# Kernel tuning notes

Hardware: AMD Instinct MI355X
Metric: run time of the kernel (lower is better)

## Reference

```python
import jax, jax.numpy as jnp
import numpy as np

NUM_CLASSES = 21
CHANNELS = 256


def setup_inputs() -> dict:
    key = jax.random.key(0)
    k1, k2 = jax.random.split(key)
    B, C, Hf, Wf = 16, CHANNELS, 128, 128
    Hl, Wl = 512, 512
    features = jax.random.normal(k1, (B, C, Hf, Wf), dtype=jnp.float32)
    labels = jax.random.randint(k2, (B, Hl, Wl), 0, NUM_CLASSES, dtype=jnp.int64)
    return {"features": features, "labels": labels}


def _nearest_resize_labels(labels, Hf, Wf):
    # torch F.interpolate(mode='nearest'): src = floor(dst * in/out)
    B, Hl, Wl = labels.shape
    ih = (jnp.arange(Hf) * Hl) // Hf  # [Hf]
    iw = (jnp.arange(Wf) * Wl) // Wf  # [Wf]
    return labels[:, ih[:, None], iw[None, :]]  # [B, Hf, Wf]


def reference(features, labels):
    B, C, Hf, Wf = features.shape
    lab = _nearest_resize_labels(labels, Hf, Wf)  # [B,Hf,Wf] int
    seg = lab.reshape(-1)  # [B*Hf*Wf]
    feats = features.transpose(0, 2, 3, 1).reshape(-1, C)  # [B*Hf*Wf, C]
    # segment-mean over classes: sums and counts in one fused pass each
    sums = jax.ops.segment_sum(feats, seg, num_segments=NUM_CLASSES)  # [K, C]
    counts = jax.ops.segment_sum(jnp.ones((seg.shape[0],), dtype=feats.dtype), seg,
                                 num_segments=NUM_CLASSES)  # [K]
    protos = sums / jnp.maximum(counts, 1.0)[:, None]
    # classes absent from the batch produce no proto (dict omission in the original);
    # represent as zeros here, with counts signalling validity
    protos = jnp.where(counts[:, None] > 0, protos, jnp.zeros_like(protos))
    return protos, counts
```

## Files before the change

kernel.cpp:

```cpp
#include <hip/hip_runtime.h>
#include <hip/hip_bf16.h>

#define NUM_CLASSES 21
#define CHANNELS 256
#define B_SZ 16
#define HF 128
#define WF 128
#define HL 512
#define WL 512
#define PIX_PER_BLOCK 512
#define TILES_PER_B (HF * WF / PIX_PER_BLOCK)
#define PCHUNK 64
#define NCHUNK (PIX_PER_BLOCK / PCHUNK)
#define FPAD 65

__global__ __launch_bounds__(256) void protos_accum_kernel(
    const float* __restrict__ feats,
    const int*   __restrict__ labels,
    float* __restrict__ sums,
    int*   __restrict__ counts)
{
    __shared__ float fbuf[CHANNELS * FPAD];
    __shared__ int   lbl[PIX_PER_BLOCK];
    __shared__ int   cnt[NUM_CLASSES];

    const int t    = threadIdx.x;
    const int lane = t & 63;
    const int b    = blockIdx.x >> 5;
    const int tile = blockIdx.x & 31;
    const int base = tile * PIX_PER_BLOCK;

    if (t < NUM_CLASSES) cnt[t] = 0;

    const int p0 = base + 2 * t;
    const int h0 = p0 >> 7,       w0 = p0 & 127;
    const int h1 = (p0 + 1) >> 7, w1 = (p0 + 1) & 127;
    const int l0 = labels[(size_t)b * (HL * WL) + (size_t)(h0 * 4) * WL + w0 * 4];
    const int l1 = labels[(size_t)b * (HL * WL) + (size_t)(h1 * 4) * WL + w1 * 4];
    lbl[2 * t]     = l0;
    lbl[2 * t + 1] = l1;
    __syncthreads();
    atomicAdd(&cnt[l0], 1);
    atomicAdd(&cnt[l1], 1);

    float acc[NUM_CLASSES];
    #pragma unroll
    for (int k = 0; k < NUM_CLASSES; ++k) acc[k] = 0.0f;

    const float* fb = feats + (size_t)b * CHANNELS * (HF * WF);

    for (int chk = 0; chk < NCHUNK; ++chk) {
        const int pbase = base + chk * PCHUNK;

        float4 v[16];
        #pragma unroll
        for (int i = 0; i < 16; ++i) {
            const int flat = i * 256 + t;
            const int c = flat >> 4;
            const int q = flat & 15;
            v[i] = *(const float4*)(fb + (size_t)c * (HF * WF) + pbase + q * 4);
        }
        __syncthreads();

        #pragma unroll
        for (int i = 0; i < 16; ++i) {
            const int flat = i * 256 + t;
            const int c = flat >> 4;
            const int q = flat & 15;
            float* d = &fbuf[c * FPAD + q * 4];
            d[0] = v[i].x; d[1] = v[i].y; d[2] = v[i].z; d[3] = v[i].w;
        }
        __syncthreads();

        const int mylbl = lbl[chk * PCHUNK + lane];
        const float* frow = &fbuf[t * FPAD];

        #pragma unroll 8
        for (int p = 0; p < PCHUNK; ++p) {
            const float vv = frow[p];
            const int lb = __builtin_amdgcn_readlane(mylbl, p);
            switch (lb) {
                case 0:  acc[0]  += vv; break;
                case 1:  acc[1]  += vv; break;
                case 2:  acc[2]  += vv; break;
                case 3:  acc[3]  += vv; break;
                case 4:  acc[4]  += vv; break;
                case 5:  acc[5]  += vv; break;
                case 6:  acc[6]  += vv; break;
                case 7:  acc[7]  += vv; break;
                case 8:  acc[8]  += vv; break;
                case 9:  acc[9]  += vv; break;
                case 10: acc[10] += vv; break;
                case 11: acc[11] += vv; break;
                case 12: acc[12] += vv; break;
                case 13: acc[13] += vv; break;
                case 14: acc[14] += vv; break;
                case 15: acc[15] += vv; break;
                case 16: acc[16] += vv; break;
                case 17: acc[17] += vv; break;
                case 18: acc[18] += vv; break;
                case 19: acc[19] += vv; break;
                case 20: acc[20] += vv; break;
                default: break;
            }
        }
    }

    #pragma unroll
    for (int k = 0; k < NUM_CLASSES; ++k)
        unsafeAtomicAdd(&sums[k * CHANNELS + t], acc[k]);
    if (t < NUM_CLASSES) atomicAdd(&counts[t], cnt[t]);
}

__global__ __launch_bounds__(256) void protos_finalize_kernel(
    const float* __restrict__ sums,
    const int*   __restrict__ counts,
    float* __restrict__ out)
{
    const int k = blockIdx.x;
    const int c = threadIdx.x;
    const float cn = (float)counts[k];
    const float p = (cn > 0.0f) ? (sums[k * CHANNELS + c] / fmaxf(cn, 1.0f)) : 0.0f;
    out[k * CHANNELS + c] = p;
    if (c == 0) out[NUM_CLASSES * CHANNELS + k] = cn;
}

extern "C" void kernel_launch(void* const* d_in, const int* in_sizes, int n_in,
                              void* d_out, int out_size, void* d_ws, size_t ws_size,
                              hipStream_t stream) {
    const float* feats  = (const float*)d_in[0];
    const int*   labels = (const int*)d_in[1];
    float* sums   = (float*)d_ws;
    int*   counts = (int*)(sums + NUM_CLASSES * CHANNELS);
    float* out    = (float*)d_out;

    hipMemsetAsync(d_ws, 0,
                   (NUM_CLASSES * CHANNELS) * sizeof(float) + NUM_CLASSES * sizeof(int),
                   stream);

    dim3 grid(B_SZ * TILES_PER_B);
    dim3 block(256);
    protos_accum_kernel<<<grid, block, 0, stream>>>(feats, labels, sums, counts);

    protos_finalize_kernel<<<dim3(NUM_CLASSES), dim3(CHANNELS), 0, stream>>>(sums, counts, out);
}
```

Before: 412.1 us.

## Prefetch next feature chunk into registers and use ballot-based class accumulation

Feature loads for the next 64-pixel chunk are issued into registers before the current chunk is processed, so global memory latency overlaps with accumulation. The per-pixel jump-table switch is replaced by a per-class ballot mask: the kernel walks the set bits and sums the matching LDS values, and popcount of the mask gives the class counts. This removes the shared-memory atomic histogram. The cost is longer register live ranges, from the held prefetch buffer plus the per-class count array, and an extra barrier per chunk.

```diff
diff --git a/kernel.cpp b/kernel.cpp
--- a/kernel.cpp
+++ b/kernel.cpp
@@ -14,6 +14,17 @@
 #define NCHUNK (PIX_PER_BLOCK / PCHUNK)
 #define FPAD 65
 
+__device__ __forceinline__ void load_chunk(const float* __restrict__ fb, int pbase, int t,
+                                           float4* __restrict__ v) {
+    #pragma unroll
+    for (int i = 0; i < 16; ++i) {
+        const int flat = i * 256 + t;
+        const int c = flat >> 4;
+        const int q = flat & 15;
+        v[i] = *(const float4*)(fb + (size_t)c * (HF * WF) + pbase + q * 4);
+    }
+}
+
 __global__ __launch_bounds__(256) void protos_accum_kernel(
     const float* __restrict__ feats,
     const int*   __restrict__ labels,
@@ -22,7 +33,6 @@
 {
     __shared__ float fbuf[CHANNELS * FPAD];
     __shared__ int   lbl[PIX_PER_BLOCK];
-    __shared__ int   cnt[NUM_CLASSES];
 
     const int t    = threadIdx.x;
     const int lane = t & 63;
@@ -30,38 +40,25 @@
     const int tile = blockIdx.x & 31;
     const int base = tile * PIX_PER_BLOCK;
 
-    if (t < NUM_CLASSES) cnt[t] = 0;
-
-    const int p0 = base + 2 * t;
-    const int h0 = p0 >> 7,       w0 = p0 & 127;
-    const int h1 = (p0 + 1) >> 7, w1 = (p0 + 1) & 127;
-    const int l0 = labels[(size_t)b * (HL * WL) + (size_t)(h0 * 4) * WL + w0 * 4];
-    const int l1 = labels[(size_t)b * (HL * WL) + (size_t)(h1 * 4) * WL + w1 * 4];
-    lbl[2 * t]     = l0;
-    lbl[2 * t + 1] = l1;
-    __syncthreads();
-    atomicAdd(&cnt[l0], 1);
-    atomicAdd(&cnt[l1], 1);
+    {
+        const int p0 = base + 2 * t;
+        const int h0 = p0 >> 7,       w0 = p0 & 127;
+        const int h1 = (p0 + 1) >> 7, w1 = (p0 + 1) & 127;
+        lbl[2 * t]     = labels[(size_t)b * (HL * WL) + (size_t)(h0 * 4) * WL + w0 * 4];
+        lbl[2 * t + 1] = labels[(size_t)b * (HL * WL) + (size_t)(h1 * 4) * WL + w1 * 4];
+    }
 
     float acc[NUM_CLASSES];
+    int   scnt[NUM_CLASSES];
     #pragma unroll
-    for (int k = 0; k < NUM_CLASSES; ++k) acc[k] = 0.0f;
+    for (int k = 0; k < NUM_CLASSES; ++k) { acc[k] = 0.0f; scnt[k] = 0; }
 
     const float* fb = feats + (size_t)b * CHANNELS * (HF * WF);
 
+    float4 v[16];
+    load_chunk(fb, base, t, v);
+
     for (int chk = 0; chk < NCHUNK; ++chk) {
-        const int pbase = base + chk * PCHUNK;
-
-        float4 v[16];
-        #pragma unroll
-        for (int i = 0; i < 16; ++i) {
-            const int flat = i * 256 + t;
-            const int c = flat >> 4;
-            const int q = flat & 15;
-            v[i] = *(const float4*)(fb + (size_t)c * (HF * WF) + pbase + q * 4);
-        }
-        __syncthreads();
-
         #pragma unroll
         for (int i = 0; i < 16; ++i) {
             const int flat = i * 256 + t;
@@ -72,44 +69,36 @@
         }
         __syncthreads();
 
+        if (chk + 1 < NCHUNK)
+            load_chunk(fb, base + (chk + 1) * PCHUNK, t, v);
+
         const int mylbl = lbl[chk * PCHUNK + lane];
         const float* frow = &fbuf[t * FPAD];
 
-        #pragma unroll 8
-        for (int p = 0; p < PCHUNK; ++p) {
-            const float vv = frow[p];
-            const int lb = __builtin_amdgcn_readlane(mylbl, p);
-            switch (lb) {
-                case 0:  acc[0]  += vv; break;
-                case 1:  acc[1]  += vv; break;
-                case 2:  acc[2]  += vv; break;
-                case 3:  acc[3]  += vv; break;
-                case 4:  acc[4]  += vv; break;
-                case 5:  acc[5]  += vv; break;
-                case 6:  acc[6]  += vv; break;
-                case 7:  acc[7]  += vv; break;
-                case 8:  acc[8]  += vv; break;
-                case 9:  acc[9]  += vv; break;
-                case 10: acc[10] += vv; break;
-                case 11: acc[11] += vv; break;
-                case 12: acc[12] += vv; break;
-                case 13: acc[13] += vv; break;
-                case 14: acc[14] += vv; break;
-                case 15: acc[15] += vv; break;
-                case 16: acc[16] += vv; break;
-                case 17: acc[17] += vv; break;
-                case 18: acc[18] += vv; break;
-                case 19: acc[19] += vv; break;
-                case 20: acc[20] += vv; break;
-                default: break;
+        #pragma unroll
+        for (int k = 0; k < NUM_CLASSES; ++k) {
+            unsigned long long m = __ballot(mylbl == k);
+            scnt[k] += (int)__popcll(m);
+            float s = 0.0f;
+            while (m) {
+                const int p = (int)__builtin_ctzll(m);
+                m &= (m - 1);
+                s += frow[p];
             }
+            acc[k] += s;
         }
+        __syncthreads();
     }
 
     #pragma unroll
     for (int k = 0; k < NUM_CLASSES; ++k)
         unsafeAtomicAdd(&sums[k * CHANNELS + t], acc[k]);
-    if (t < NUM_CLASSES) atomicAdd(&counts[t], cnt[t]);
+
+    if (t == 0) {
+        #pragma unroll
+        for (int k = 0; k < NUM_CLASSES; ++k)
+            atomicAdd(&counts[k], scnt[k]);
+    }
 }
 
 __global__ __launch_bounds__(256) void protos_finalize_kernel(
```

Result: slower. 439.2 us (+6.6%).
